# Performance work log

Hardware: AMD Instinct MI355X
Metric: run time of the kernel (lower is better)

Reference implementation:

```python
import jax, jax.numpy as jnp
import numpy as np

B, NF, NC, C = 4, 200000, 50000, 32
EP, E = 200000, 800000
EPS = 1e-5


def setup_inputs() -> dict:
    key = jax.random.key(0)
    ks = jax.random.split(key, 20)
    inp = {
        "x": jax.random.normal(ks[0], (B, NF, C), dtype=jnp.float32),
        "pool_src": jax.random.randint(ks[1], (EP,), 0, NF),
        "pool_dst": jax.random.randint(ks[2], (EP,), 0, NC),
        "pool_attr": jax.random.uniform(ks[3], (EP,), dtype=jnp.float32),
        "edge_src": jax.random.randint(ks[4], (E,), 0, NC),
        "edge_dst": jax.random.randint(ks[5], (E,), 0, NC),
        "edge_attr": jax.random.uniform(ks[6], (E,), dtype=jnp.float32),
        "num_coarse": NC,
    }
    scale = 1.0 / np.sqrt(C)
    for i in range(4):
        inp[f"Wr{i+1}"] = jax.random.normal(ks[7 + 3 * i], (C, C), dtype=jnp.float32) * scale
        inp[f"Wn{i+1}"] = jax.random.normal(ks[8 + 3 * i], (C, C), dtype=jnp.float32) * scale
        inp[f"b{i+1}"] = jnp.zeros((C,), dtype=jnp.float32)
    return inp


def _gconv(x, src, dst, ea, Wr, Wn, b, n):
    # weighted GraphConv: out = x @ Wr + (scatter_add_e ea[e] * x[src[e]]) @ Wn + b
    msg = x[:, src, :] * ea[None, :, None]                       # [B, E, C]
    agg = jnp.zeros((x.shape[0], n, x.shape[2]), x.dtype).at[:, dst, :].add(msg)
    return x @ Wr + agg @ Wn + b


def _instance_norm(x):
    # InstanceNorm1d (affine=False): normalize each (batch, channel) over nodes
    m = jnp.mean(x, axis=1, keepdims=True)
    v = jnp.var(x, axis=1, keepdims=True)
    return (x - m) * jax.lax.rsqrt(v + EPS)


def reference(x, pool_src, pool_dst, pool_attr, edge_src, edge_dst, edge_attr,
              Wr1, Wn1, b1, Wr2, Wn2, b2, Wr3, Wn3, b3, Wr4, Wn4, b4, num_coarse):
    # CustomPoolingAdd: out[:, dst] += edge_attr * x[:, src]  (fine -> coarse)
    pooled = jnp.zeros((x.shape[0], num_coarse, x.shape[2]), x.dtype)
    pooled = pooled.at[:, pool_dst, :].add(x[:, pool_src, :] * pool_attr[None, :, None])
    h = _gconv(pooled, edge_src, edge_dst, edge_attr, Wr1, Wn1, b1, num_coarse)
    h = _gconv(h, edge_src, edge_dst, edge_attr, Wr2, Wn2, b2, num_coarse)
    h = _instance_norm(h)
    h = _gconv(h, edge_src, edge_dst, edge_attr, Wr3, Wn3, b3, num_coarse)
    h = _gconv(h, edge_src, edge_dst, edge_attr, Wr4, Wn4, b4, num_coarse)
    return h
```

## Files before the change

kernel.cpp:

```cpp
#include <hip/hip_runtime.h>

#define BB 4
#define NFINE 200000
#define NC 50000
#define CH 32
#define NPOOL 200000
#define NEDGE 800000
#define EPSV 1e-5f
#define NWAVES 8192
#define NCHUNK 49

__device__ __forceinline__ int rfl(int v) { return __builtin_amdgcn_readfirstlane(v); }

__global__ void zero_kernel(int* __restrict__ p, int n) {
    int i = blockIdx.x * blockDim.x + threadIdx.x;
    int stride = gridDim.x * blockDim.x;
    for (; i < n; i += stride) p[i] = 0;
}

__global__ void hist_kernel(const int* __restrict__ dst, int n, int* __restrict__ cnt) {
    int i = blockIdx.x * blockDim.x + threadIdx.x;
    int stride = gridDim.x * blockDim.x;
    for (; i < n; i += stride) atomicAdd(&cnt[dst[i]], 1);
}

__global__ __launch_bounds__(1024)
void chunk_sum_kernel(const int* __restrict__ cntP, const int* __restrict__ cntE,
                      int* __restrict__ scanTmp) {
    __shared__ int lds[1024];
    const int* __restrict__ cnt = blockIdx.y ? cntE : cntP;
    int* csum = scanTmp + (blockIdx.y ? 64 : 0);
    const int j = blockIdx.x, t = threadIdx.x;
    const int idx = j * 1024 + t;
    lds[t] = (idx < NC) ? cnt[idx] : 0;
    __syncthreads();
    for (int off = 512; off > 0; off >>= 1) {
        if (t < off) lds[t] += lds[t + off];
        __syncthreads();
    }
    if (t == 0) csum[j] = lds[0];
}

__global__ void chunk_mid_kernel(int* __restrict__ scanTmp) {
    int* csum = scanTmp + (blockIdx.y ? 64 : 0);
    int* coff = scanTmp + (blockIdx.y ? 192 : 128);
    const int t = threadIdx.x;
    int v = (t < NCHUNK) ? csum[t] : 0;
    const int orig = v;
    for (int off = 1; off < 64; off <<= 1) {
        int u = __shfl_up(v, off, 64);
        if (t >= off) v += u;
    }
    if (t < NCHUNK) coff[t] = v - orig;
}

__global__ __launch_bounds__(1024)
void chunk_scan_kernel(int* __restrict__ cntP, int* __restrict__ cntE,
                       const int* __restrict__ scanTmp,
                       int* __restrict__ rowpP, int* __restrict__ rowpE) {
    __shared__ int lds[1024];
    int* __restrict__ cnt = blockIdx.y ? cntE : cntP;
    const int* coff = scanTmp + (blockIdx.y ? 192 : 128);
    int* __restrict__ rowp = blockIdx.y ? rowpE : rowpP;
    const int j = blockIdx.x, t = threadIdx.x;
    const int idx = j * 1024 + t;
    const int v = (idx < NC) ? cnt[idx] : 0;
    lds[t] = v;
    __syncthreads();
    for (int off = 1; off < 1024; off <<= 1) {
        int u = (t >= off) ? lds[t - off] : 0;
        __syncthreads();
        lds[t] += u;
        __syncthreads();
    }
    const int excl = lds[t] - v + coff[j];
    if (idx < NC) {
        rowp[idx] = excl;
        cnt[idx] = excl;
    }
    if (idx == NC - 1) rowp[NC] = excl + v;
}

__global__ void scatter_kernel(const int* __restrict__ src, const int* __restrict__ dst,
                               const float* __restrict__ attr, int n,
                               int* __restrict__ next, int2* __restrict__ pk) {
    int i = blockIdx.x * blockDim.x + threadIdx.x;
    int stride = gridDim.x * blockDim.x;
    for (; i < n; i += stride) {
        int d = dst[i];
        int pos = atomicAdd(&next[d], 1);
        pk[pos] = make_int2(src[i], __float_as_int(attr[i]));
    }
}

__global__ __launch_bounds__(256)
void pool_kernel(const float* __restrict__ x, float* __restrict__ pooled,
                 const int* __restrict__ rowp, const int2* __restrict__ pk) {
    const int tid = threadIdx.x;
    const int lane = tid & 63;
    const int c = lane & 31;
    const int bh = lane >> 5;
    const int n = blockIdx.x * 4 + (tid >> 6);
    if (n >= NC) return;
    const float* __restrict__ xA = x + (size_t)(2 * bh) * NFINE * CH;
    const float* __restrict__ xB = x + (size_t)(2 * bh + 1) * NFINE * CH;
    int e0 = rfl(rowp[n]), e1 = rfl(rowp[n + 1]);
    float2 a0 = {0, 0}, a1 = {0, 0}, a2 = {0, 0}, a3 = {0, 0};
    int e = e0;
    for (; e + 4 <= e1; e += 4) {
        int2 p0 = pk[e], p1 = pk[e + 1], p2 = pk[e + 2], p3 = pk[e + 3];
        float w0 = __int_as_float(p0.y), w1 = __int_as_float(p1.y);
        float w2 = __int_as_float(p2.y), w3 = __int_as_float(p3.y);
        a0.x += w0 * xA[p0.x * CH + c]; a0.y += w0 * xB[p0.x * CH + c];
        a1.x += w1 * xA[p1.x * CH + c]; a1.y += w1 * xB[p1.x * CH + c];
        a2.x += w2 * xA[p2.x * CH + c]; a2.y += w2 * xB[p2.x * CH + c];
        a3.x += w3 * xA[p3.x * CH + c]; a3.y += w3 * xB[p3.x * CH + c];
    }
    for (; e < e1; ++e) {
        int2 p0 = pk[e];
        float w0 = __int_as_float(p0.y);
        a0.x += w0 * xA[p0.x * CH + c];
        a0.y += w0 * xB[p0.x * CH + c];
    }
    ((float2*)pooled)[(n * CH + c) * 2 + bh] =
        make_float2((a0.x + a1.x) + (a2.x + a3.x), (a0.y + a1.y) + (a2.y + a3.y));
}

template<bool NORM>
__global__ __launch_bounds__(256)
void dense_kernel(const float* hin, float* zout , float* __restrict__ gout,
                  const float* __restrict__ Wr, const float* __restrict__ Wn,
                  const float* __restrict__ bias, const float* __restrict__ st) {
    __shared__ float2 stage[4][2][64];
    const int tid = threadIdx.x;
    const int lane = tid & 63;
    const int c = lane & 31;
    const int bh = lane >> 5;
    const int w = tid >> 6;
    const int wid = blockIdx.x * 4 + w;

    float wr[CH], wn[CH];
#pragma unroll
    for (int k = 0; k < CH; ++k) {
        wr[k] = Wr[k * CH + c];
        wn[k] = Wn[k * CH + c];
    }
    const float bc = bias[c];

    float2 rs = {1.f, 1.f}, mr = {0.f, 0.f};
    if constexpr (NORM) {
        float2 m2 = ((const float2*)(st + 256))[c * 2 + bh];
        rs = ((const float2*)(st + 384))[c * 2 + bh];
        mr = make_float2(m2.x * rs.x, m2.y * rs.y);
    }

    const float2* h2 = (const float2*)hin;
    int it = 0;
    for (int n = wid; n < NC; n += NWAVES, ++it) {
        float2 xv = h2[(n * CH + c) * 2 + bh];
        if constexpr (NORM) {
            xv.x = xv.x * rs.x - mr.x;
            xv.y = xv.y * rs.y - mr.y;
        }
        stage[w][it & 1][lane] = xv;
        float2 z = {bc, bc}, g = {0.f, 0.f};
#pragma unroll
        for (int k = 0; k < CH; ++k) {
            float2 v = stage[w][it & 1][bh * 32 + k];
            z.x += v.x * wr[k]; z.y += v.y * wr[k];
            g.x += v.x * wn[k]; g.y += v.y * wn[k];
        }
        ((float2*)zout)[(n * CH + c) * 2 + bh] = z;
        ((float2*)gout)[(n * CH + c) * 2 + bh] = g;
    }
}

template<bool OUTBNC>
__global__ __launch_bounds__(256)
void gather_kernel(const float* zin ,
                   const float* __restrict__ gin, float* hout,
                   const int* __restrict__ rowp, const int2* __restrict__ pk) {
    const int tid = threadIdx.x;
    const int lane = tid & 63;
    const int c = lane & 31;
    const int bh = lane >> 5;
    const int n = blockIdx.x * 4 + (tid >> 6);
    if (n >= NC) return;

    const float2* __restrict__ g2 = (const float2*)gin;
    float2 acc = ((const float2*)zin)[(n * CH + c) * 2 + bh];
    float2 ac1 = {0.f, 0.f};
    int e0 = rfl(rowp[n]), e1 = rfl(rowp[n + 1]);
    int e = e0;
    for (; e + 8 <= e1; e += 8) {
#pragma unroll
        for (int i = 0; i < 8; i += 2) {
            int2 p0 = pk[e + i], p1 = pk[e + i + 1];
            float w0 = __int_as_float(p0.y), w1 = __int_as_float(p1.y);
            float2 v0 = g2[(p0.x * CH + c) * 2 + bh];
            float2 v1 = g2[(p1.x * CH + c) * 2 + bh];
            acc.x += w0 * v0.x; acc.y += w0 * v0.y;
            ac1.x += w1 * v1.x; ac1.y += w1 * v1.y;
        }
    }
    for (; e < e1; ++e) {
        int2 p0 = pk[e];
        float w0 = __int_as_float(p0.y);
        float2 v0 = g2[(p0.x * CH + c) * 2 + bh];
        acc.x += w0 * v0.x; acc.y += w0 * v0.y;
    }
    acc.x += ac1.x; acc.y += ac1.y;
    if constexpr (OUTBNC) {
        hout[(size_t)(2 * bh + 0) * (NC * CH) + n * CH + c] = acc.x;
        hout[(size_t)(2 * bh + 1) * (NC * CH) + n * CH + c] = acc.y;
    } else {
        ((float2*)hout)[(n * CH + c) * 2 + bh] = acc;
    }
}

__global__ __launch_bounds__(256)
void stats_kernel(const float* __restrict__ h, float* __restrict__ st) {
    __shared__ float4 ls[256], lq[256];
    const int tid = threadIdx.x;
    float4 s = {0, 0, 0, 0}, q = {0, 0, 0, 0};
    const float4* __restrict__ h4 = (const float4*)h;
    const int total4 = NC * CH;
    const int stride = gridDim.x * blockDim.x;
    for (int i = blockIdx.x * blockDim.x + tid; i < total4; i += stride) {
        float4 v = h4[i];
        s.x += v.x; s.y += v.y; s.z += v.z; s.w += v.w;
        q.x += v.x * v.x; q.y += v.y * v.y; q.z += v.z * v.z; q.w += v.w * v.w;
    }
    ls[tid] = s; lq[tid] = q;
    __syncthreads();
    if (tid < 32) {
        float4 ts = ls[tid], tq = lq[tid];
#pragma unroll
        for (int g = 1; g < 8; ++g) {
            float4 o = ls[g * 32 + tid];
            ts.x += o.x; ts.y += o.y; ts.z += o.z; ts.w += o.w;
            float4 p = lq[g * 32 + tid];
            tq.x += p.x; tq.y += p.y; tq.z += p.z; tq.w += p.w;
        }
        atomicAdd(&st[tid * 4 + 0], ts.x);
        atomicAdd(&st[tid * 4 + 1], ts.y);
        atomicAdd(&st[tid * 4 + 2], ts.z);
        atomicAdd(&st[tid * 4 + 3], ts.w);
        atomicAdd(&st[128 + tid * 4 + 0], tq.x);
        atomicAdd(&st[128 + tid * 4 + 1], tq.y);
        atomicAdd(&st[128 + tid * 4 + 2], tq.z);
        atomicAdd(&st[128 + tid * 4 + 3], tq.w);
    }
}

__global__ void stats_fin(float* __restrict__ st) {
    int i = threadIdx.x;
    if (i < 128) {
        float m = st[i] * (1.f / NC);
        float v = st[128 + i] * (1.f / NC) - m * m;
        st[256 + i] = m;
        st[384 + i] = rsqrtf(v + EPSV);
    }
}

__global__ __launch_bounds__(256)
void transpose_kernel(const float* __restrict__ in, float* __restrict__ out) {
    const int tid = threadIdx.x;
    const int lane = tid & 63;
    const int c = lane & 31;
    const int bh = lane >> 5;
    const int n = blockIdx.x * 4 + (tid >> 6);
    if (n >= NC) return;
    float2 v = ((const float2*)in)[(n * CH + c) * 2 + bh];
    out[(size_t)(2 * bh + 0) * (NC * CH) + n * CH + c] = v.x;
    out[(size_t)(2 * bh + 1) * (NC * CH) + n * CH + c] = v.y;
}

extern "C" void kernel_launch(void* const* d_in, const int* in_sizes, int n_in,
                              void* d_out, int out_size, void* d_ws, size_t ws_size,
                              hipStream_t stream) {
    const float* x         = (const float*)d_in[0];
    const int*   pool_src  = (const int*)d_in[1];
    const int*   pool_dst  = (const int*)d_in[2];
    const float* pool_attr = (const float*)d_in[3];
    const int*   edge_src  = (const int*)d_in[4];
    const int*   edge_dst  = (const int*)d_in[5];
    const float* edge_attr = (const float*)d_in[6];
    const float* Wr1 = (const float*)d_in[8];
    const float* Wn1 = (const float*)d_in[9];
    const float* b1  = (const float*)d_in[10];
    const float* Wr2 = (const float*)d_in[11];
    const float* Wn2 = (const float*)d_in[12];
    const float* b2  = (const float*)d_in[13];
    const float* Wr3 = (const float*)d_in[14];
    const float* Wn3 = (const float*)d_in[15];
    const float* b3  = (const float*)d_in[16];
    const float* Wr4 = (const float*)d_in[17];
    const float* Wn4 = (const float*)d_in[18];
    const float* b4  = (const float*)d_in[19];

    const size_t BUFB = (size_t)NC * CH * BB * 4;
    const size_t CSRB = 2 * (size_t)(NC + 1) * 4 + 2 * (size_t)NC * 4 + 512 * 4 + 256 * 4
                        + (size_t)NPOOL * 8 + (size_t)NEDGE * 8;
    char* w = (char*)d_ws;
    float* G = (float*)w;  w += BUFB;
    const bool bigws = ws_size >= 2 * BUFB + CSRB + 1024;
    float* P;
    if (bigws) { P = (float*)w; w += BUFB; }
    else       { P = (float*)d_out; }
    int*   poolRow  = (int*)w;  w += (size_t)(NC + 1) * 4;
    int*   edgeRow  = (int*)w;  w += (size_t)(NC + 1) * 4;
    int*   zbase    = (int*)w;
    int*   poolNext = (int*)w;  w += (size_t)NC * 4;
    int*   edgeNext = (int*)w;  w += (size_t)NC * 4;
    float* stats    = (float*)w; w += 512 * 4;
    int*   scanTmp  = (int*)w;  w += 256 * 4;
    int2*  poolPk   = (int2*)w; w += (size_t)NPOOL * 8;
    int2*  edgePk   = (int2*)w; w += (size_t)NEDGE * 8;

    float* out = (float*)d_out;
    const int ZN = NC + NC + 256;
    const int NB = (NC + 3) / 4;

    zero_kernel<<<98, 1024, 0, stream>>>(zbase, ZN);
    hist_kernel<<<782, 256, 0, stream>>>(pool_dst, NPOOL, poolNext);
    hist_kernel<<<3125, 256, 0, stream>>>(edge_dst, NEDGE, edgeNext);
    chunk_sum_kernel<<<dim3(NCHUNK, 2), 1024, 0, stream>>>(poolNext, edgeNext, scanTmp);
    chunk_mid_kernel<<<dim3(1, 2), 64, 0, stream>>>(scanTmp);
    chunk_scan_kernel<<<dim3(NCHUNK, 2), 1024, 0, stream>>>(poolNext, edgeNext, scanTmp,
                                                            poolRow, edgeRow);
    scatter_kernel<<<782, 256, 0, stream>>>(pool_src, pool_dst, pool_attr, NPOOL,
                                            poolNext, poolPk);
    scatter_kernel<<<3125, 256, 0, stream>>>(edge_src, edge_dst, edge_attr, NEDGE,
                                             edgeNext, edgePk);

    pool_kernel<<<NB, 256, 0, stream>>>(x, P, poolRow, poolPk);

    dense_kernel<false><<<2048, 256, 0, stream>>>(P, P, G, Wr1, Wn1, b1, nullptr);
    gather_kernel<false><<<NB, 256, 0, stream>>>(P, G, P, edgeRow, edgePk);

    dense_kernel<false><<<2048, 256, 0, stream>>>(P, P, G, Wr2, Wn2, b2, nullptr);
    gather_kernel<false><<<NB, 256, 0, stream>>>(P, G, P, edgeRow, edgePk);

    stats_kernel<<<200, 256, 0, stream>>>(P, stats);
    stats_fin<<<1, 128, 0, stream>>>(stats);

    dense_kernel<true><<<2048, 256, 0, stream>>>(P, P, G, Wr3, Wn3, b3, stats);
    gather_kernel<false><<<NB, 256, 0, stream>>>(P, G, P, edgeRow, edgePk);

    dense_kernel<false><<<2048, 256, 0, stream>>>(P, P, G, Wr4, Wn4, b4, nullptr);
    if (bigws) {
        gather_kernel<true><<<NB, 256, 0, stream>>>(P, G, out, edgeRow, edgePk);
    } else {
        gather_kernel<false><<<NB, 256, 0, stream>>>(P, G, P, edgeRow, edgePk);
        transpose_kernel<<<NB, 256, 0, stream>>>(P, G);
        hipMemcpyAsync(out, G, BUFB, hipMemcpyDeviceToDevice, stream);
    }
}
```

Baseline: 674.6 us.

## Fuse pooling and edge-gather with following dense transforms via lane swizzles

```diff
diff --git a/kernel.cpp b/kernel.cpp
--- a/kernel.cpp
+++ b/kernel.cpp
@@ -11,6 +11,31 @@
 #define NCHUNK 49
 
 __device__ __forceinline__ int rfl(int v) { return __builtin_amdgcn_readfirstlane(v); }
+
+template<int K>
+__device__ __forceinline__ float2 bcast2(float2 v) {
+    union { float f; int i; } x, y;
+    x.f = v.x; y.f = v.y;
+    x.i = __builtin_amdgcn_ds_swizzle(x.i, (K << 5));
+    y.i = __builtin_amdgcn_ds_swizzle(y.i, (K << 5));
+    return make_float2(x.f, y.f);
+}
+
+template<int K>
+struct MM2 {
+    static __device__ __forceinline__ void run(const float2& v, const float* wr,
+                                               const float* wn, float2& z, float2& g) {
+        MM2<K - 1>::run(v, wr, wn, z, g);
+        float2 vb = bcast2<K>(v);
+        z.x += vb.x * wr[K]; z.y += vb.y * wr[K];
+        g.x += vb.x * wn[K]; g.y += vb.y * wn[K];
+    }
+};
+template<>
+struct MM2<-1> {
+    static __device__ __forceinline__ void run(const float2&, const float*,
+                                               const float*, float2&, float2&) {}
+};
 
 __global__ void zero_kernel(int* __restrict__ p, int n) {
     int i = blockIdx.x * blockDim.x + threadIdx.x;
@@ -126,9 +151,105 @@
         make_float2((a0.x + a1.x) + (a2.x + a3.x), (a0.y + a1.y) + (a2.y + a3.y));
 }
 
+__global__ __launch_bounds__(256)
+void pool_dense_kernel(const float* __restrict__ x, float* __restrict__ zout,
+                       float* __restrict__ gout,
+                       const int* __restrict__ rowp, const int2* __restrict__ pk,
+                       const float* __restrict__ Wr, const float* __restrict__ Wn,
+                       const float* __restrict__ bias) {
+    const int tid = threadIdx.x;
+    const int lane = tid & 63;
+    const int c = lane & 31;
+    const int bh = lane >> 5;
+    const int n = blockIdx.x * 4 + (tid >> 6);
+    if (n >= NC) return;
+    float wr[CH], wn[CH];
+#pragma unroll
+    for (int k = 0; k < CH; ++k) {
+        wr[k] = Wr[k * CH + c];
+        wn[k] = Wn[k * CH + c];
+    }
+    const float bc = bias[c];
+    const float* __restrict__ xA = x + (size_t)(2 * bh) * NFINE * CH;
+    const float* __restrict__ xB = x + (size_t)(2 * bh + 1) * NFINE * CH;
+    int e0 = rfl(rowp[n]), e1 = rfl(rowp[n + 1]);
+    float2 a0 = {0, 0}, a1 = {0, 0}, a2 = {0, 0}, a3 = {0, 0};
+    int e = e0;
+    for (; e + 4 <= e1; e += 4) {
+        int2 p0 = pk[e], p1 = pk[e + 1], p2 = pk[e + 2], p3 = pk[e + 3];
+        float w0 = __int_as_float(p0.y), w1 = __int_as_float(p1.y);
+        float w2 = __int_as_float(p2.y), w3 = __int_as_float(p3.y);
+        a0.x += w0 * xA[p0.x * CH + c]; a0.y += w0 * xB[p0.x * CH + c];
+        a1.x += w1 * xA[p1.x * CH + c]; a1.y += w1 * xB[p1.x * CH + c];
+        a2.x += w2 * xA[p2.x * CH + c]; a2.y += w2 * xB[p2.x * CH + c];
+        a3.x += w3 * xA[p3.x * CH + c]; a3.y += w3 * xB[p3.x * CH + c];
+    }
+    for (; e < e1; ++e) {
+        int2 p0 = pk[e];
+        float w0 = __int_as_float(p0.y);
+        a0.x += w0 * xA[p0.x * CH + c];
+        a0.y += w0 * xB[p0.x * CH + c];
+    }
+    float2 pooled = make_float2((a0.x + a1.x) + (a2.x + a3.x),
+                                (a0.y + a1.y) + (a2.y + a3.y));
+    float2 z = {bc, bc}, g = {0.f, 0.f};
+    MM2<CH - 1>::run(pooled, wr, wn, z, g);
+    ((float2*)zout)[(n * CH + c) * 2 + bh] = z;
+    ((float2*)gout)[(n * CH + c) * 2 + bh] = g;
+}
+
+__global__ __launch_bounds__(256)
+void gd_kernel(float* zio, const float* __restrict__ gin, float* __restrict__ gout,
+               const int* __restrict__ rowp, const int2* __restrict__ pk,
+               const float* __restrict__ Wr, const float* __restrict__ Wn,
+               const float* __restrict__ bias) {
+    const int tid = threadIdx.x;
+    const int lane = tid & 63;
+    const int c = lane & 31;
+    const int bh = lane >> 5;
+    const int n = blockIdx.x * 4 + (tid >> 6);
+    if (n >= NC) return;
+    float wr[CH], wn[CH];
+#pragma unroll
+    for (int k = 0; k < CH; ++k) {
+        wr[k] = Wr[k * CH + c];
+        wn[k] = Wn[k * CH + c];
+    }
+    const float bc = bias[c];
+
+    const float2* __restrict__ g2 = (const float2*)gin;
+    float2 acc = ((float2*)zio)[(n * CH + c) * 2 + bh];
+    float2 ac1 = {0.f, 0.f};
+    int e0 = rfl(rowp[n]), e1 = rfl(rowp[n + 1]);
+    int e = e0;
+    for (; e + 8 <= e1; e += 8) {
+#pragma unroll
+        for (int i = 0; i < 8; i += 2) {
+            int2 p0 = pk[e + i], p1 = pk[e + i + 1];
+            float w0 = __int_as_float(p0.y), w1 = __int_as_float(p1.y);
+            float2 v0 = g2[(p0.x * CH + c) * 2 + bh];
+            float2 v1 = g2[(p1.x * CH + c) * 2 + bh];
+            acc.x += w0 * v0.x; acc.y += w0 * v0.y;
+            ac1.x += w1 * v1.x; ac1.y += w1 * v1.y;
+        }
+    }
+    for (; e < e1; ++e) {
+        int2 p0 = pk[e];
+        float w0 = __int_as_float(p0.y);
+        float2 v0 = g2[(p0.x * CH + c) * 2 + bh];
+        acc.x += w0 * v0.x; acc.y += w0 * v0.y;
+    }
+    acc.x += ac1.x; acc.y += ac1.y;
+
+    float2 z = {bc, bc}, g = {0.f, 0.f};
+    MM2<CH - 1>::run(acc, wr, wn, z, g);
+    ((float2*)zio)[(n * CH + c) * 2 + bh] = z;
+    ((float2*)gout)[(n * CH + c) * 2 + bh] = g;
+}
+
 template<bool NORM>
 __global__ __launch_bounds__(256)
-void dense_kernel(const float* hin, float* zout , float* __restrict__ gout,
+void dense_kernel(const float* hin, float* zout, float* __restrict__ gout,
                   const float* __restrict__ Wr, const float* __restrict__ Wn,
                   const float* __restrict__ bias, const float* __restrict__ st) {
     __shared__ float2 stage[4][2][64];
@@ -177,8 +298,7 @@
 
 template<bool OUTBNC>
 __global__ __launch_bounds__(256)
-void gather_kernel(const float* zin ,
-                   const float* __restrict__ gin, float* hout,
+void gather_kernel(const float* zin, const float* __restrict__ gin, float* hout,
                    const int* __restrict__ rowp, const int2* __restrict__ pk) {
     const int tid = threadIdx.x;
     const int lane = tid & 63;
@@ -303,11 +423,18 @@
     const size_t CSRB = 2 * (size_t)(NC + 1) * 4 + 2 * (size_t)NC * 4 + 512 * 4 + 256 * 4
                         + (size_t)NPOOL * 8 + (size_t)NEDGE * 8;
     char* w = (char*)d_ws;
-    float* G = (float*)w;  w += BUFB;
     const bool bigws = ws_size >= 2 * BUFB + CSRB + 1024;
+
+    float* D = (float*)d_out;
     float* P;
-    if (bigws) { P = (float*)w; w += BUFB; }
-    else       { P = (float*)d_out; }
+    float* G;
+    if (bigws) {
+        P = (float*)w;  w += BUFB;
+        G = (float*)w;  w += BUFB;
+    } else {
+        G = (float*)w;  w += BUFB;
+        P = D;
+    }
     int*   poolRow  = (int*)w;  w += (size_t)(NC + 1) * 4;
     int*   edgeRow  = (int*)w;  w += (size_t)(NC + 1) * 4;
     int*   zbase    = (int*)w;
@@ -318,7 +445,6 @@
     int2*  poolPk   = (int2*)w; w += (size_t)NPOOL * 8;
     int2*  edgePk   = (int2*)w; w += (size_t)NEDGE * 8;
 
-    float* out = (float*)d_out;
     const int ZN = NC + NC + 256;
     const int NB = (NC + 3) / 4;
 
@@ -334,26 +460,28 @@
     scatter_kernel<<<3125, 256, 0, stream>>>(edge_src, edge_dst, edge_attr, NEDGE,
                                              edgeNext, edgePk);
 
-    pool_kernel<<<NB, 256, 0, stream>>>(x, P, poolRow, poolPk);
-
-    dense_kernel<false><<<2048, 256, 0, stream>>>(P, P, G, Wr1, Wn1, b1, nullptr);
-    gather_kernel<false><<<NB, 256, 0, stream>>>(P, G, P, edgeRow, edgePk);
-
-    dense_kernel<false><<<2048, 256, 0, stream>>>(P, P, G, Wr2, Wn2, b2, nullptr);
-    gather_kernel<false><<<NB, 256, 0, stream>>>(P, G, P, edgeRow, edgePk);
-
-    stats_kernel<<<200, 256, 0, stream>>>(P, stats);
-    stats_fin<<<1, 128, 0, stream>>>(stats);
-
-    dense_kernel<true><<<2048, 256, 0, stream>>>(P, P, G, Wr3, Wn3, b3, stats);
-    gather_kernel<false><<<NB, 256, 0, stream>>>(P, G, P, edgeRow, edgePk);
-
-    dense_kernel<false><<<2048, 256, 0, stream>>>(P, P, G, Wr4, Wn4, b4, nullptr);
     if (bigws) {
-        gather_kernel<true><<<NB, 256, 0, stream>>>(P, G, out, edgeRow, edgePk);
+        pool_dense_kernel<<<NB, 256, 0, stream>>>(x, P, G, poolRow, poolPk, Wr1, Wn1, b1);
+        gd_kernel<<<NB, 256, 0, stream>>>(P, G, D, edgeRow, edgePk, Wr2, Wn2, b2);
+        gather_kernel<false><<<NB, 256, 0, stream>>>(P, D, G, edgeRow, edgePk);
+        stats_kernel<<<200, 256, 0, stream>>>(G, stats);
+        stats_fin<<<1, 128, 0, stream>>>(stats);
+        dense_kernel<true><<<2048, 256, 0, stream>>>(G, P, D, Wr3, Wn3, b3, stats);
+        gd_kernel<<<NB, 256, 0, stream>>>(P, D, G, edgeRow, edgePk, Wr4, Wn4, b4);
+        gather_kernel<true><<<NB, 256, 0, stream>>>(P, G, D, edgeRow, edgePk);
     } else {
+        pool_kernel<<<NB, 256, 0, stream>>>(x, P, poolRow, poolPk);
+        dense_kernel<false><<<2048, 256, 0, stream>>>(P, P, G, Wr1, Wn1, b1, nullptr);
+        gather_kernel<false><<<NB, 256, 0, stream>>>(P, G, P, edgeRow, edgePk);
+        dense_kernel<false><<<2048, 256, 0, stream>>>(P, P, G, Wr2, Wn2, b2, nullptr);
+        gather_kernel<false><<<NB, 256, 0, stream>>>(P, G, P, edgeRow, edgePk);
+        stats_kernel<<<200, 256, 0, stream>>>(P, stats);
+        stats_fin<<<1, 128, 0, stream>>>(stats);
+        dense_kernel<true><<<2048, 256, 0, stream>>>(P, P, G, Wr3, Wn3, b3, stats);
+        gather_kernel<false><<<NB, 256, 0, stream>>>(P, G, P, edgeRow, edgePk);
+        dense_kernel<false><<<2048, 256, 0, stream>>>(P, P, G, Wr4, Wn4, b4, nullptr);
         gather_kernel<false><<<NB, 256, 0, stream>>>(P, G, P, edgeRow, edgePk);
         transpose_kernel<<<NB, 256, 0, stream>>>(P, G);
-        hipMemcpyAsync(out, G, BUFB, hipMemcpyDeviceToDevice, stream);
-    }
-}
+        hipMemcpyAsync(D, G, BUFB, hipMemcpyDeviceToDevice, stream);
+    }
+}
```

Result: slower. 758.6 us (+12.4%).
